# Performance work log

Hardware: AMD Instinct MI355X
Metric: run time of the kernel (lower is better)

Reference implementation:

```python
import jax, jax.numpy as jnp
import numpy as np

N = 50_000      # node_num
E = 1_600_000   # n_edges (avg degree 32)
D = 256         # input feature dim
H = 128         # GCN / hidden units
FC = 1024       # fc0 units
C = 16          # num_classes


def _tn(key, shape, std=0.1):
    # truncated normal in [-2, 2] std, matching tf.random.truncated_normal(stddev=0.1)
    return jax.random.truncated_normal(key, -2.0, 2.0, shape, jnp.float32) * std


def setup_inputs() -> dict:
    key = jax.random.key(0)
    ks = jax.random.split(key, 16)
    return {
        "x": jax.random.normal(ks[0], (N, D), jnp.float32),
        "edge_index": jax.random.randint(ks[1], (2, E), 0, N, jnp.int32),
        # GCN layer params (tfg GCN: kernel + bias)
        "gcn0_W": _tn(ks[2], (D, H)), "gcn0_b": jnp.zeros((H,), jnp.float32),
        "gcn1_W": _tn(ks[3], (H, H)), "gcn1_b": jnp.zeros((H,), jnp.float32),
        "gcn2_W": _tn(ks[4], (H, H)), "gcn2_b": jnp.zeros((H,), jnp.float32),
        # extra dense block between gcn10 and gcn11
        "w1": _tn(ks[5], (H, H)), "b1": _tn(ks[6], (N, H)),
        # fc head
        "fc0_W": _tn(ks[7], (H, FC)), "fc0_b": jnp.zeros((FC,), jnp.float32),
        "fc1_W": _tn(ks[8], (FC, C)), "fc1_b": jnp.zeros((C,), jnp.float32),
    }


def reference(x, edge_index, gcn0_W, gcn0_b, gcn1_W, gcn1_b, gcn2_W, gcn2_b,
              w1, b1, fc0_W, fc0_b, fc1_W, fc1_b):
    n = x.shape[0]
    src, dst = edge_index[0], edge_index[1]
    loops = jnp.arange(n, dtype=src.dtype)
    # GCN renormalization trick: A_hat = A + I, w_ij = deg_i^-1/2 * deg_j^-1/2
    src_f = jnp.concatenate([src, loops])   # [E+N]
    dst_f = jnp.concatenate([dst, loops])
    deg = jax.ops.segment_sum(jnp.ones(src_f.shape[0], jnp.float32), src_f, num_segments=n)
    norm = jnp.where(deg > 0, deg, 1.0) ** -0.5
    ew = norm[src_f] * norm[dst_f]          # [E+N]

    def gcn(h, W, b):
        h = h @ W                                                      # [N,H]
        agg = jax.ops.segment_sum(h[src_f] * ew[:, None], dst_f, num_segments=n)
        return agg + b

    h1 = jax.nn.relu(gcn(x, gcn0_W, gcn0_b))       # gcn10, relu
    h11 = jax.nn.relu(h1 @ w1 + b1)                # dense with per-node bias
    h2 = gcn(h11, gcn1_W, gcn1_b)                  # gcn11, no activation
    h2 = jax.nn.relu(gcn(h2, gcn2_W, gcn2_b))      # gcn12, relu
    h = h1 + h2
    h = jax.nn.relu(h @ fc0_W + fc0_b)             # fc0
    return h @ fc1_W + fc1_b                       # fc1 logits [N,C]
```

## Files before the change

### kernel.cpp

```cpp
#include <hip/hip_runtime.h>
#include <hip/hip_bf16.h>
#include <hip/hip_fp16.h>
#include <cstddef>
#include <cstdint>

#define NNODES 50000
#define NEDGES 1600000
#define DIM 256
#define HID 128
#define FCU 1024
#define NCLS 16

#define NBKT 256
#define BW 196
#define NBLK_A 64
#define EPB (NEDGES / NBLK_A)
#define CAPB 8192

typedef short s16x8 __attribute__((ext_vector_type(8)));
typedef _Float16 f16x8 __attribute__((ext_vector_type(8)));
typedef float f32x4 __attribute__((ext_vector_type(4)));
#define MFMA16 __builtin_amdgcn_mfma_f32_16x16x32_bf16
#define MFMAH  __builtin_amdgcn_mfma_f32_16x16x32_f16

typedef unsigned short u16;
typedef unsigned int u32;

__device__ inline u16 f2bf(float f) {
    u32 u = __float_as_uint(f);
    return (u16)((u + 0x7FFF + ((u >> 16) & 1)) >> 16);
}
__device__ inline float bf2f(u16 h) { return __uint_as_float(((u32)h) << 16); }
__device__ inline void split2(float v, u16& h, u16& l) {
    h = f2bf(v);
    l = f2bf(v - bf2f(h));
}


__global__ void count_kernel(const int* __restrict__ ei, int* __restrict__ degS) {
    int e = blockIdx.x * blockDim.x + threadIdx.x;
    if (e < NEDGES) atomicAdd(&degS[ei[e]], 1);
}

__global__ void norm_kernel(const int* __restrict__ degS, float* __restrict__ nrm) {
    int i = blockIdx.x * blockDim.x + threadIdx.x;
    if (i < NNODES) nrm[i] = rsqrtf((float)(degS[i] + 1));
}

__global__ __launch_bounds__(1024) void histA(const int* __restrict__ ei, int* __restrict__ hist) {
    __shared__ int h[NBKT];
    int blk = blockIdx.x, t = threadIdx.x;
    if (t < NBKT) h[t] = 0;
    __syncthreads();
    int base = blk * EPB;
    for (int e = base + t; e < base + EPB; e += 1024) {
        int dst = ei[NEDGES + e];
        atomicAdd(&h[dst / BW], 1);
    }
    __syncthreads();
    if (t < NBKT) hist[t * NBLK_A + blk] = h[t];
}

__global__ __launch_bounds__(1024) void scanh_a(int* __restrict__ hist, int* __restrict__ bsum) {
    __shared__ int s[1024];
    int b = blockIdx.x, t = threadIdx.x, i = b * 1024 + t;
    int v = hist[i];
    s[t] = v;
    __syncthreads();
    for (int off = 1; off < 1024; off <<= 1) {
        int x = (t >= off) ? s[t - off] : 0;
        __syncthreads();
        s[t] += x;
        __syncthreads();
    }
    hist[i] = s[t] - v;
    if (t == 1023) bsum[b] = s[1023];
}
__global__ void scanh_b(int* __restrict__ bsum) {
    if (threadIdx.x == 0 && blockIdx.x == 0) {
        int a = 0;
        for (int j = 0; j < 16; ++j) { int t = bsum[j]; bsum[j] = a; a += t; }
    }
}
__global__ __launch_bounds__(1024) void scanh_c(int* __restrict__ hist, const int* __restrict__ bsum) {
    int i = blockIdx.x * 1024 + threadIdx.x;
    hist[i] += bsum[blockIdx.x];
}

__global__ __launch_bounds__(1024) void bucket_fill(const int* __restrict__ ei,
                                                    const int* __restrict__ hist,
                                                    u32* __restrict__ packed) {
    __shared__ int cur[NBKT];
    int blk = blockIdx.x, t = threadIdx.x;
    if (t < NBKT) cur[t] = hist[t * NBLK_A + blk];
    __syncthreads();
    int base = blk * EPB;
    for (int e = base + t; e < base + EPB; e += 1024) {
        int src = ei[e], dst = ei[NEDGES + e];
        int p = atomicAdd(&cur[dst / BW], 1);
        packed[p] = ((u32)dst << 16) | (u32)src;
    }
}

__global__ __launch_bounds__(256) void bucket_csr(const u32* __restrict__ packed,
                                                  const int* __restrict__ hist,
                                                  int* __restrict__ rowptr, u16* __restrict__ csr) {
    __shared__ u32 st[CAPB];
    __shared__ u16 so[CAPB];
    __shared__ int cnt[256], excl[256];
    int b = blockIdx.x, t = threadIdx.x;
    int ebase = hist[b * NBLK_A];
    int eend  = (b < NBKT - 1) ? hist[(b + 1) * NBLK_A] : NEDGES;
    int nE = eend - ebase;
    if (nE > CAPB) nE = CAPB;
    cnt[t] = 0;
    __syncthreads();
    for (int i = t; i < nE; i += 256) {
        u32 p = packed[ebase + i];
        st[i] = p;
        atomicAdd(&cnt[(int)(p >> 16) - b * BW], 1);
    }
    __syncthreads();
    int v = cnt[t];
    excl[t] = v;
    __syncthreads();
    for (int off = 1; off < 256; off <<= 1) {
        int x = (t >= off) ? excl[t - off] : 0;
        __syncthreads();
        excl[t] += x;
        __syncthreads();
    }
    int ex = excl[t] - v;
    int node = b * BW + t;
    if (t < BW && node < NNODES) rowptr[node] = ebase + ex;
    if (b == NBKT - 1 && t == 0) rowptr[NNODES] = NEDGES;
    cnt[t] = ex;
    __syncthreads();
    for (int i = t; i < nE; i += 256) {
        u32 p = st[i];
        int pos = atomicAdd(&cnt[(int)(p >> 16) - b * BW], 1);
        so[pos] = (u16)(p & 0xFFFF);
    }
    __syncthreads();
    for (int i = t; i < nE; i += 256) csr[ebase + i] = so[i];
}


__global__ __launch_bounds__(256) void conv_x(const float* __restrict__ x,
                                              u16* __restrict__ xh, u16* __restrict__ xl) {
    int i = blockIdx.x * blockDim.x + threadIdx.x;
    const float4 v = *reinterpret_cast<const float4*>(x + (size_t)i * 4);
    u16 h0, l0, h1, l1, h2, l2, h3, l3;
    split2(v.x, h0, l0); split2(v.y, h1, l1); split2(v.z, h2, l2); split2(v.w, h3, l3);
    ushort4 hv = make_ushort4(h0, h1, h2, h3), lv = make_ushort4(l0, l1, l2, l3);
    *reinterpret_cast<ushort4*>(xh + (size_t)i * 4) = hv;
    *reinterpret_cast<ushort4*>(xl + (size_t)i * 4) = lv;
}

__global__ __launch_bounds__(256) void conv_wT(const float* __restrict__ W, int K, int N,
                                               u16* __restrict__ outH, u16* __restrict__ outL) {
    int o = blockIdx.x * blockDim.x + threadIdx.x;
    if (o < K * N) {
        int n = o / K, k = o - n * K;
        u16 h, l;
        split2(W[(size_t)k * N + n], h, l);
        outH[o] = h; outL[o] = l;
    }
}

__global__ __launch_bounds__(256) void conv_w1h(const float* __restrict__ W, __half* __restrict__ outT) {
    int o = blockIdx.x * blockDim.x + threadIdx.x;
    if (o < FCU * NCLS) {
        int n = o / FCU, k = o - n * FCU;
        outT[o] = __float2half(W[(size_t)k * NCLS + n]);
    }
}


template<int VAR>
__global__ __launch_bounds__(256) void agg_fast(
    const __half* __restrict__ g, const float* __restrict__ nrm,
    const int* __restrict__ rowptr, const u16* __restrict__ csr,
    const float* __restrict__ bias,
    const u16* __restrict__ h1H, const u16* __restrict__ h1L,
    u16* __restrict__ outH, u16* __restrict__ outL)
{
    int w = threadIdx.x >> 6, lane = threadIdx.x & 63;
    int i = blockIdx.x * 4 + w;
    if (i >= NNODES) return;
    const __half2* gp = reinterpret_cast<const __half2*>(g);
    size_t lrow = (size_t)i * 64 + lane;
    float2 acc = __half22float2(gp[lrow]);
    int e0 = rowptr[i], e1 = rowptr[i + 1];
    int e = e0;
    for (; e + 8 <= e1; e += 8) {
        int s[8];
#pragma unroll
        for (int q = 0; q < 8; ++q) s[q] = csr[e + q];
        __half2 v[8];
#pragma unroll
        for (int q = 0; q < 8; ++q) v[q] = gp[(size_t)s[q] * 64 + lane];
#pragma unroll
        for (int q = 0; q < 8; ++q) {
            float2 f = __half22float2(v[q]);
            acc.x += f.x; acc.y += f.y;
        }
    }
    for (; e < e1; ++e) {
        int s = csr[e];
        float2 f = __half22float2(gp[(size_t)s * 64 + lane]);
        acc.x += f.x; acc.y += f.y;
    }
    float ni = nrm[i];
    const float2 b = *reinterpret_cast<const float2*>(bias + lane * 2);
    float v0 = fmaf(ni, acc.x, b.x);
    float v1 = fmaf(ni, acc.y, b.y);
    if (VAR != 1) { v0 = fmaxf(v0, 0.f); v1 = fmaxf(v1, 0.f); }
    if (VAR == 2) {
        ushort2 rh = *reinterpret_cast<const ushort2*>(h1H + (size_t)i * HID + lane * 2);
        ushort2 rl = *reinterpret_cast<const ushort2*>(h1L + (size_t)i * HID + lane * 2);
        v0 += bf2f(rh.x) + bf2f(rl.x);
        v1 += bf2f(rh.y) + bf2f(rl.y);
    }
    u16 h0, l0, h1v, l1v;
    split2(v0, h0, l0);
    split2(v1, h1v, l1v);
    *reinterpret_cast<ushort2*>(outH + (size_t)i * HID + lane * 2) = make_ushort2(h0, h1v);
    *reinterpret_cast<ushort2*>(outL + (size_t)i * HID + lane * 2) = make_ushort2(l0, l1v);
}


template<int K, int MODE>
__global__ __launch_bounds__(256) void gemm_split(
    const u16* __restrict__ Ah, const u16* __restrict__ Al,
    const u16* __restrict__ BTh, const u16* __restrict__ BTl,
    const float* __restrict__ pnb, const float* __restrict__ nrmv,
    __half* __restrict__ outG, u16* __restrict__ outH, u16* __restrict__ outL, int M)
{
    const int PK = 40;
    __shared__ __align__(16) u16 AsH[64 * PK], AsL[64 * PK];
    __shared__ __align__(16) u16 BsH[128 * PK], BsL[128 * PK];
    int tid = threadIdx.x, lane = tid & 63, w = tid >> 6;
    int wr = w >> 1, wc = w & 1;
    int l15 = lane & 15, l4 = lane >> 4;
    int blockRow = blockIdx.x * 64;
    f32x4 acc[2][4] = {};

    for (int kk = 0; kk < K; kk += 32) {
        {
            int row = tid >> 2, kc = (tid & 3) * 8;
            int gr = blockRow + row; if (gr >= M) gr = M - 1;
            *(s16x8*)&AsH[row * PK + kc] = *(const s16x8*)&Ah[(size_t)gr * K + kk + kc];
            *(s16x8*)&AsL[row * PK + kc] = *(const s16x8*)&Al[(size_t)gr * K + kk + kc];
        }
#pragma unroll
        for (int i2 = 0; i2 < 2; ++i2) {
            int idx = tid + i2 * 256;
            int n = idx >> 2, kc = (idx & 3) * 8;
            *(s16x8*)&BsH[n * PK + kc] = *(const s16x8*)&BTh[(size_t)n * K + kk + kc];
            *(s16x8*)&BsL[n * PK + kc] = *(const s16x8*)&BTl[(size_t)n * K + kk + kc];
        }
        __syncthreads();
        s16x8 ah[2], al[2], bh[4], bl[4];
#pragma unroll
        for (int mi = 0; mi < 2; ++mi) {
            ah[mi] = *(const s16x8*)&AsH[(wr * 32 + mi * 16 + l15) * PK + 8 * l4];
            al[mi] = *(const s16x8*)&AsL[(wr * 32 + mi * 16 + l15) * PK + 8 * l4];
        }
#pragma unroll
        for (int ni = 0; ni < 4; ++ni) {
            bh[ni] = *(const s16x8*)&BsH[(wc * 64 + ni * 16 + l15) * PK + 8 * l4];
            bl[ni] = *(const s16x8*)&BsL[(wc * 64 + ni * 16 + l15) * PK + 8 * l4];
        }
#pragma unroll
        for (int mi = 0; mi < 2; ++mi)
#pragma unroll
            for (int ni = 0; ni < 4; ++ni) {
                acc[mi][ni] = MFMA16(ah[mi], bh[ni], acc[mi][ni], 0, 0, 0);
                acc[mi][ni] = MFMA16(ah[mi], bl[ni], acc[mi][ni], 0, 0, 0);
                acc[mi][ni] = MFMA16(al[mi], bh[ni], acc[mi][ni], 0, 0, 0);
            }
        __syncthreads();
    }
#pragma unroll
    for (int mi = 0; mi < 2; ++mi)
#pragma unroll
        for (int ni = 0; ni < 4; ++ni) {
            int c = wc * 64 + ni * 16 + l15;
#pragma unroll
            for (int j = 0; j < 4; ++j) {
                int r = blockRow + wr * 32 + mi * 16 + l4 * 4 + j;
                if (r < M) {
                    if (MODE == 0) {
                        outG[(size_t)r * 128 + c] = __float2half(nrmv[r] * acc[mi][ni][j]);
                    } else {
                        float v = fmaxf(acc[mi][ni][j] + pnb[(size_t)r * 128 + c], 0.f);
                        u16 h, l;
                        split2(v, h, l);
                        outH[(size_t)r * 128 + c] = h;
                        outL[(size_t)r * 128 + c] = l;
                    }
                }
            }
        }
}


__global__ __launch_bounds__(256) void fc_kernel(
    const u16* __restrict__ Ahi,
    const u16* __restrict__ BTh,
    const float* __restrict__ fc0b,
    const __half* __restrict__ W1f,
    const float* __restrict__ fc1b,
    float* __restrict__ out, int M)
{
    __shared__ __align__(16) u16 vs[64 * 128];
    __shared__ __align__(16) u16 W1s[16 * 128];
    int tid = threadIdx.x, lane = tid & 63, w = tid >> 6;
    int wr = w >> 1, wc = w & 1;
    int l15 = lane & 15, l4 = lane >> 4;
    int blockRow = blockIdx.x * 64;

    s16x8 ahr[2][4];
#pragma unroll
    for (int mi = 0; mi < 2; ++mi) {
        int r = blockRow + wr * 32 + mi * 16 + l15; if (r >= M) r = M - 1;
#pragma unroll
        for (int ks = 0; ks < 4; ++ks)
            ahr[mi][ks] = *(const s16x8*)&Ahi[(size_t)r * HID + ks * 32 + 8 * l4];
    }

    f32x4 acc2 = {0.f, 0.f, 0.f, 0.f};

    for (int cc = 0; cc < FCU / 128; ++cc) {
        int co = cc * 128;
        f32x4 acc[2][4] = {};
#pragma unroll
        for (int ks = 0; ks < 4; ++ks) {
            int kk = ks * 32;
            s16x8 bh[4];
#pragma unroll
            for (int ni = 0; ni < 4; ++ni)
                bh[ni] = *(const s16x8*)&BTh[(size_t)(co + wc * 64 + ni * 16 + l15) * HID + kk + 8 * l4];
#pragma unroll
            for (int mi = 0; mi < 2; ++mi)
#pragma unroll
                for (int ni = 0; ni < 4; ++ni)
                    acc[mi][ni] = MFMA16(ahr[mi][ks], bh[ni], acc[mi][ni], 0, 0, 0);
        }

        {
            int cls = tid >> 4, kc = (tid & 15) * 8;
            s16x8 t = *(const s16x8*)&W1f[(size_t)cls * FCU + co + kc];
            *(s16x8*)&W1s[cls * 128 + (kc ^ ((cls & 7) << 3))] = t;
        }
#pragma unroll
        for (int mi = 0; mi < 2; ++mi)
#pragma unroll
            for (int ni = 0; ni < 4; ++ni) {
                int unit = wc * 64 + ni * 16 + l15;
                float b0v = fc0b[co + unit];
#pragma unroll
                for (int j = 0; j < 4; ++j) {
                    int rl = wr * 32 + mi * 16 + l4 * 4 + j;
                    float v = fmaxf(acc[mi][ni][j] + b0v, 0.f);
                    vs[rl * 128 + (unit ^ ((rl & 7) << 3))] = __half_as_ushort(__float2half(v));
                }
            }
        __syncthreads();

#pragma unroll
        for (int ks = 0; ks < 4; ++ks) {
            int row = w * 16 + l15;
            int colk = ks * 32 + 8 * l4;
            f16x8 a2 = *(const f16x8*)&vs[row * 128 + (colk ^ ((row & 7) << 3))];
            f16x8 b2 = *(const f16x8*)&W1s[l15 * 128 + (colk ^ ((l15 & 7) << 3))];
            acc2 = MFMAH(a2, b2, acc2, 0, 0, 0);
        }
        __syncthreads();
    }

#pragma unroll
    for (int j = 0; j < 4; ++j) {
        int gr = blockRow + w * 16 + l4 * 4 + j;
        if (gr < M) out[(size_t)gr * NCLS + l15] = acc2[j] + fc1b[l15];
    }
}


extern "C" void kernel_launch(void* const* d_in, const int* in_sizes, int n_in,
                              void* d_out, int out_size, void* d_ws, size_t ws_size,
                              hipStream_t stream)
{
    const float* x     = (const float*)d_in[0];
    const int*   ei    = (const int*)d_in[1];
    const float* gcn0W = (const float*)d_in[2];
    const float* gcn0b = (const float*)d_in[3];
    const float* gcn1W = (const float*)d_in[4];
    const float* gcn1b = (const float*)d_in[5];
    const float* gcn2W = (const float*)d_in[6];
    const float* gcn2b = (const float*)d_in[7];
    const float* w1    = (const float*)d_in[8];
    const float* b1    = (const float*)d_in[9];
    const float* fc0W  = (const float*)d_in[10];
    const float* fc0b  = (const float*)d_in[11];
    const float* fc1W  = (const float*)d_in[12];
    const float* fc1b  = (const float*)d_in[13];
    float* out = (float*)d_out;

    char* ws = (char*)d_ws;
    size_t off = 0;
    auto alloc = [&](size_t bytes) -> void* {
        void* p = ws + off;
        off = (off + bytes + 255) & ~(size_t)255;
        return p;
    };
    int* degS   = (int*)alloc((size_t)NNODES * 4);
    int* rowptr = (int*)alloc((size_t)(NNODES + 1) * 4);
    int* hist   = (int*)alloc((size_t)NBKT * NBLK_A * 4);
    int* bsum   = (int*)alloc(64 * 4);
    u32* packed = (u32*)alloc((size_t)NEDGES * 4);
    u16* csr    = (u16*)alloc((size_t)NEDGES * 2);
    float* nrm  = (float*)alloc((size_t)NNODES * 4);
    u16* W0Th = (u16*)alloc((size_t)DIM * HID * 2);  u16* W0Tl = (u16*)alloc((size_t)DIM * HID * 2);
    u16* w1Th = (u16*)alloc((size_t)HID * HID * 2);  u16* w1Tl = (u16*)alloc((size_t)HID * HID * 2);
    u16* W1Th = (u16*)alloc((size_t)HID * HID * 2);  u16* W1Tl = (u16*)alloc((size_t)HID * HID * 2);
    u16* W2Th = (u16*)alloc((size_t)HID * HID * 2);  u16* W2Tl = (u16*)alloc((size_t)HID * HID * 2);
    u16* F0Th = (u16*)alloc((size_t)HID * FCU * 2);  u16* F0Tl = (u16*)alloc((size_t)HID * FCU * 2);
    __half* W1f = (__half*)alloc((size_t)FCU * NCLS * 2);
    __half* bufG = (__half*)alloc((size_t)NNODES * HID * 2);
    u16* R1 = (u16*)alloc((size_t)2 * NNODES * DIM * 2);
    u16* xh = R1, *xl = R1 + (size_t)NNODES * DIM;
    u16* h1H = R1,                            *h1L = R1 + (size_t)NNODES * HID;
    u16* B3H = R1 + (size_t)2 * NNODES * HID, *B3L = R1 + (size_t)3 * NNODES * HID;

    const int M = NNODES;
    hipMemsetAsync(degS, 0, (size_t)NNODES * 4, stream);

    count_kernel<<<(NEDGES + 255) / 256, 256, 0, stream>>>(ei, degS);
    norm_kernel<<<(NNODES + 255) / 256, 256, 0, stream>>>(degS, nrm);
    histA<<<NBLK_A, 1024, 0, stream>>>(ei, hist);
    scanh_a<<<16, 1024, 0, stream>>>(hist, bsum);
    scanh_b<<<1, 64, 0, stream>>>(bsum);
    scanh_c<<<16, 1024, 0, stream>>>(hist, bsum);
    bucket_fill<<<NBLK_A, 1024, 0, stream>>>(ei, hist, packed);
    bucket_csr<<<NBKT, 256, 0, stream>>>(packed, hist, rowptr, csr);

    conv_x<<<(NNODES * DIM / 4 + 255) / 256, 256, 0, stream>>>(x, xh, xl);
    conv_wT<<<(DIM * HID + 255) / 256, 256, 0, stream>>>(gcn0W, DIM, HID, W0Th, W0Tl);
    conv_wT<<<(HID * HID + 255) / 256, 256, 0, stream>>>(w1,    HID, HID, w1Th, w1Tl);
    conv_wT<<<(HID * HID + 255) / 256, 256, 0, stream>>>(gcn1W, HID, HID, W1Th, W1Tl);
    conv_wT<<<(HID * HID + 255) / 256, 256, 0, stream>>>(gcn2W, HID, HID, W2Th, W2Tl);
    conv_wT<<<(HID * FCU + 255) / 256, 256, 0, stream>>>(fc0W,  HID, FCU, F0Th, F0Tl);
    conv_w1h<<<(FCU * NCLS + 255) / 256, 256, 0, stream>>>(fc1W, W1f);

    const int GB = (M + 63) / 64;
    const int AB = (NNODES + 3) / 4;
    gemm_split<DIM, 0><<<GB, 256, 0, stream>>>(xh, xl, W0Th, W0Tl, nullptr, nrm, bufG, nullptr, nullptr, M);
    agg_fast<0><<<AB, 256, 0, stream>>>(bufG, nrm, rowptr, csr, gcn0b, nullptr, nullptr, h1H, h1L);
    gemm_split<HID, 1><<<GB, 256, 0, stream>>>(h1H, h1L, w1Th, w1Tl, b1, nullptr, nullptr, B3H, B3L, M);
    gemm_split<HID, 0><<<GB, 256, 0, stream>>>(B3H, B3L, W1Th, W1Tl, nullptr, nrm, bufG, nullptr, nullptr, M);
    agg_fast<1><<<AB, 256, 0, stream>>>(bufG, nrm, rowptr, csr, gcn1b, nullptr, nullptr, B3H, B3L);
    gemm_split<HID, 0><<<GB, 256, 0, stream>>>(B3H, B3L, W2Th, W2Tl, nullptr, nrm, bufG, nullptr, nullptr, M);
    agg_fast<2><<<AB, 256, 0, stream>>>(bufG, nrm, rowptr, csr, gcn2b, h1H, h1L, B3H, B3L);
    fc_kernel<<<GB, 256, 0, stream>>>(B3H, F0Th, fc0b, W1f, fc1b, out, M);
}
```

Baseline: 495.8 us.

## Retile fc kernel to 32-row blocks with register-prefetched fc0 weights

```diff
diff --git a/kernel.cpp b/kernel.cpp
--- a/kernel.cpp
+++ b/kernel.cpp
@@ -314,40 +314,49 @@
     const float* __restrict__ fc1b,
     float* __restrict__ out, int M)
 {
-    __shared__ __align__(16) u16 vs[64 * 128];
+    __shared__ __align__(16) u16 vs[32 * 128];
     __shared__ __align__(16) u16 W1s[16 * 128];
     int tid = threadIdx.x, lane = tid & 63, w = tid >> 6;
-    int wr = w >> 1, wc = w & 1;
     int l15 = lane & 15, l4 = lane >> 4;
-    int blockRow = blockIdx.x * 64;
+    int blockRow = blockIdx.x * 32;
 
     s16x8 ahr[2][4];
 #pragma unroll
     for (int mi = 0; mi < 2; ++mi) {
-        int r = blockRow + wr * 32 + mi * 16 + l15; if (r >= M) r = M - 1;
+        int r = blockRow + mi * 16 + l15; if (r >= M) r = M - 1;
 #pragma unroll
         for (int ks = 0; ks < 4; ++ks)
             ahr[mi][ks] = *(const s16x8*)&Ahi[(size_t)r * HID + ks * 32 + 8 * l4];
     }
 
     f32x4 acc2 = {0.f, 0.f, 0.f, 0.f};
-
+    s16x8 bcur[2][4];
+#pragma unroll
+    for (int ni = 0; ni < 2; ++ni)
+#pragma unroll
+        for (int ks = 0; ks < 4; ++ks)
+            bcur[ni][ks] = *(const s16x8*)&BTh[(size_t)(w * 32 + ni * 16 + l15) * HID + ks * 32 + 8 * l4];
+
+#pragma unroll
     for (int cc = 0; cc < FCU / 128; ++cc) {
         int co = cc * 128;
-        f32x4 acc[2][4] = {};
-#pragma unroll
-        for (int ks = 0; ks < 4; ++ks) {
-            int kk = ks * 32;
-            s16x8 bh[4];
-#pragma unroll
-            for (int ni = 0; ni < 4; ++ni)
-                bh[ni] = *(const s16x8*)&BTh[(size_t)(co + wc * 64 + ni * 16 + l15) * HID + kk + 8 * l4];
+        s16x8 bnxt[2][4];
+        if (cc + 1 < FCU / 128) {
+#pragma unroll
+            for (int ni = 0; ni < 2; ++ni)
+#pragma unroll
+                for (int ks = 0; ks < 4; ++ks)
+                    bnxt[ni][ks] = *(const s16x8*)&BTh[(size_t)(co + 128 + w * 32 + ni * 16 + l15) * HID + ks * 32 + 8 * l4];
+        }
+
+        f32x4 acc[2][2] = {};
+#pragma unroll
+        for (int ks = 0; ks < 4; ++ks)
 #pragma unroll
             for (int mi = 0; mi < 2; ++mi)
 #pragma unroll
-                for (int ni = 0; ni < 4; ++ni)
-                    acc[mi][ni] = MFMA16(ahr[mi][ks], bh[ni], acc[mi][ni], 0, 0, 0);
-        }
+                for (int ni = 0; ni < 2; ++ni)
+                    acc[mi][ni] = MFMA16(ahr[mi][ks], bcur[ni][ks], acc[mi][ni], 0, 0, 0);
 
         {
             int cls = tid >> 4, kc = (tid & 15) * 8;
@@ -357,33 +366,45 @@
 #pragma unroll
         for (int mi = 0; mi < 2; ++mi)
 #pragma unroll
-            for (int ni = 0; ni < 4; ++ni) {
-                int unit = wc * 64 + ni * 16 + l15;
+            for (int ni = 0; ni < 2; ++ni) {
+                int unit = w * 32 + ni * 16 + l15;
                 float b0v = fc0b[co + unit];
 #pragma unroll
                 for (int j = 0; j < 4; ++j) {
-                    int rl = wr * 32 + mi * 16 + l4 * 4 + j;
+                    int rl = mi * 16 + l4 * 4 + j;
                     float v = fmaxf(acc[mi][ni][j] + b0v, 0.f);
                     vs[rl * 128 + (unit ^ ((rl & 7) << 3))] = __half_as_ushort(__float2half(v));
                 }
             }
         __syncthreads();
 
-#pragma unroll
-        for (int ks = 0; ks < 4; ++ks) {
-            int row = w * 16 + l15;
-            int colk = ks * 32 + 8 * l4;
-            f16x8 a2 = *(const f16x8*)&vs[row * 128 + (colk ^ ((row & 7) << 3))];
-            f16x8 b2 = *(const f16x8*)&W1s[l15 * 128 + (colk ^ ((l15 & 7) << 3))];
-            acc2 = MFMAH(a2, b2, acc2, 0, 0, 0);
-        }
-        __syncthreads();
-    }
-
-#pragma unroll
-    for (int j = 0; j < 4; ++j) {
-        int gr = blockRow + w * 16 + l4 * 4 + j;
-        if (gr < M) out[(size_t)gr * NCLS + l15] = acc2[j] + fc1b[l15];
+        if (w < 2) {
+#pragma unroll
+            for (int ks = 0; ks < 4; ++ks) {
+                int row = w * 16 + l15;
+                int colk = ks * 32 + 8 * l4;
+                f16x8 a2 = *(const f16x8*)&vs[row * 128 + (colk ^ ((row & 7) << 3))];
+                f16x8 b2 = *(const f16x8*)&W1s[l15 * 128 + (colk ^ ((l15 & 7) << 3))];
+                acc2 = MFMAH(a2, b2, acc2, 0, 0, 0);
+            }
+        }
+        __syncthreads();
+
+        if (cc + 1 < FCU / 128) {
+#pragma unroll
+            for (int ni = 0; ni < 2; ++ni)
+#pragma unroll
+                for (int ks = 0; ks < 4; ++ks)
+                    bcur[ni][ks] = bnxt[ni][ks];
+        }
+    }
+
+    if (w < 2) {
+#pragma unroll
+        for (int j = 0; j < 4; ++j) {
+            int gr = blockRow + w * 16 + l4 * 4 + j;
+            if (gr < M) out[(size_t)gr * NCLS + l15] = acc2[j] + fc1b[l15];
+        }
     }
 }
 
@@ -455,6 +476,7 @@
     conv_w1h<<<(FCU * NCLS + 255) / 256, 256, 0, stream>>>(fc1W, W1f);
 
     const int GB = (M + 63) / 64;
+    const int GB32 = (M + 31) / 32;
     const int AB = (NNODES + 3) / 4;
     gemm_split<DIM, 0><<<GB, 256, 0, stream>>>(xh, xl, W0Th, W0Tl, nullptr, nrm, bufG, nullptr, nullptr, M);
     agg_fast<0><<<AB, 256, 0, stream>>>(bufG, nrm, rowptr, csr, gcn0b, nullptr, nullptr, h1H, h1L);
@@ -463,5 +485,5 @@
     agg_fast<1><<<AB, 256, 0, stream>>>(bufG, nrm, rowptr, csr, gcn1b, nullptr, nullptr, B3H, B3L);
     gemm_split<HID, 0><<<GB, 256, 0, stream>>>(B3H, B3L, W2Th, W2Tl, nullptr, nrm, bufG, nullptr, nullptr, M);
     agg_fast<2><<<AB, 256, 0, stream>>>(bufG, nrm, rowptr, csr, gcn2b, h1H, h1L, B3H, B3L);
-    fc_kernel<<<GB, 256, 0, stream>>>(B3H, F0Th, fc0b, W1f, fc1b, out, M);
-}
+    fc_kernel<<<GB32, 256, 0, stream>>>(B3H, F0Th, fc0b, W1f, fc1b, out, M);
+}
```

After: 473.4 us. 4.5% less time.
